# Performance work log

Measured on AMD Instinct MI355X. Metric: run time of the kernel, lower is better.

The kernel has to match this reference:

```python
import jax, jax.numpy as jnp
import numpy as np

B = 262144      # points per batch
DIM = 3         # input_dim
L = 16          # levels
T = 19          # log2 hash table size
F = 2           # features per level
N_MIN, N_MAX = 16, 512

_b = np.exp((np.log(N_MAX) - np.log(N_MIN)) / (L - 1))
RES = np.floor(N_MIN * _b ** np.arange(L)).astype(np.float32).reshape(1, 1, L, 1)

# voxel corner offsets [1, DIM, 1, 2^DIM]
_border = np.empty((DIM, 2 ** DIM), dtype=np.uint32)
for i in range(DIM):
    _border[i, :] = np.array(([0] * 2 ** i + [1] * 2 ** i) * 2 ** (DIM - i - 1), dtype=np.uint32)
BORDER = _border.reshape(1, DIM, 1, 2 ** DIM)

# tiny-cuda-nn hash primes; all fit in uint32. Since the torch code takes the
# result mod 2^T (a power of two), int64 and uint32 arithmetic agree on the
# low bits, so uint32 hashing is bit-exact with the original.
PRIMES = np.array([1, 2654435761, 805459861], dtype=np.uint32)
MASK = np.uint32(2 ** T - 1)


def setup_inputs() -> dict:
    key = jax.random.key(0)
    k1, k2 = jax.random.split(key)
    x = jax.random.uniform(k1, (B, DIM), dtype=jnp.float32)  # coords in [0,1)
    tables = jax.random.uniform(k2, (L, 2 ** T, F), dtype=jnp.float32,
                                minval=-1e-4, maxval=1e-4)
    return {"x": x, "tables": tables}


def reference(x, tables):
    res = jnp.asarray(RES)                                   # [1,1,L,1]
    border = jnp.asarray(BORDER)                             # [1,DIM,1,2^DIM]
    primes = jnp.asarray(PRIMES)
    scaled = x[:, :, None, None] * res                       # [B,DIM,L,1]
    grid = jnp.floor(scaled).astype(jnp.uint32) + border     # [B,DIM,L,2^DIM]
    # spatial hash: xor of per-dim coord * prime, mod 2^T
    h = (grid[:, 0] * primes[0]) ^ (grid[:, 1] * primes[1]) ^ (grid[:, 2] * primes[2])
    idx = (h & MASK).astype(jnp.int32)                       # [B,L,2^DIM]
    gathered = tables[jnp.arange(L)[None, :, None], idx]     # [B,L,2^DIM,F]
    # multilinear interpolation weights
    w = jnp.prod(1.0 - jnp.abs(scaled - grid.astype(scaled.dtype)), axis=1)  # [B,L,2^DIM]
    out = jnp.einsum('blv,blvf->blf', w, gathered)           # [B,L,F]
    return out.reshape(x.shape[0], L * F)
```

## Files before the change

### kernel.cpp

```cpp
#include <hip/hip_runtime.h>


#define NB 262144
#define NL 16
#define TSIZE (1u << 19)
#define TMASK ((1u << 19) - 1u)
#define P1 2654435761u
#define P2 805459861u
#define NBKT 32768

typedef float vf2 __attribute__((ext_vector_type(2)));
typedef float vf4 __attribute__((ext_vector_type(4)));

__constant__ float RES_C[NL] = {16.f, 20.f, 25.f, 32.f, 40.f, 50.f, 64.f, 80.f,
                                101.f, 128.f, 161.f, 203.f, 256.f, 322.f, 406.f, 512.f};

__constant__ int SEQ_C[NL] = {0, 15, 1, 14, 2, 13, 3, 12, 4, 11, 5, 10, 6, 9, 7, 8};

__device__ __forceinline__ int bucket_of(float px, float py, float pz) {
  int bx = min(31, (int)(px * 32.0f));
  int by = min(31, (int)(py * 32.0f));
  int bz = min(31, (int)(pz * 32.0f));
  return bx | (by << 5) | (bz << 10);
}

__device__ __forceinline__ void ngp_point_level(
    float px, float py, float pz, int l, const float* __restrict__ tables,
    float& o0, float& o1) {
  const float res = RES_C[l];
  const float sx = px * res, sy = py * res, sz = pz * res;
  const float fx = floorf(sx), fy = floorf(sy), fz = floorf(sz);
  const unsigned ix = (unsigned)fx, iy = (unsigned)fy, iz = (unsigned)fz;

  const unsigned hx0 = ix, hx1 = ix + 1u;
  const unsigned hy0 = iy * P1, hy1 = hy0 + P1;
  const unsigned hz0 = iz * P2, hz1 = hz0 + P2;

  const float wx0 = 1.0f - fabsf(sx - fx);
  const float wx1 = 1.0f - fabsf(sx - (fx + 1.0f));
  const float wy0 = 1.0f - fabsf(sy - fy);
  const float wy1 = 1.0f - fabsf(sy - (fy + 1.0f));
  const float wz0 = 1.0f - fabsf(sz - fz);
  const float wz1 = 1.0f - fabsf(sz - (fz + 1.0f));

  const vf2* __restrict__ tbl = (const vf2*)tables + (size_t)l * TSIZE;

  unsigned idxs[8];
#pragma unroll
  for (int v = 0; v < 8; ++v) {
    const unsigned hx = (v & 1) ? hx1 : hx0;
    const unsigned hy = (v & 2) ? hy1 : hy0;
    const unsigned hz = (v & 4) ? hz1 : hz0;
    idxs[v] = (hx ^ hy ^ hz) & TMASK;
  }
  vf2 g[8];
#pragma unroll
  for (int v = 0; v < 8; ++v) g[v] = tbl[idxs[v]];

  o0 = 0.0f; o1 = 0.0f;
#pragma unroll
  for (int v = 0; v < 8; ++v) {
    const float w = ((v & 1) ? wx1 : wx0) * ((v & 2) ? wy1 : wy0) * ((v & 4) ? wz1 : wz0);
    o0 = fmaf(w, g[v].x, o0);
    o1 = fmaf(w, g[v].y, o1);
  }
}

__global__ __launch_bounds__(256) void zero_kernel(unsigned* __restrict__ hist) {
  hist[blockIdx.x * 256 + threadIdx.x] = 0u;
}

__global__ __launch_bounds__(256) void hist_kernel(
    const float* __restrict__ x, unsigned* __restrict__ hist) {
  const int b = blockIdx.x * 256 + threadIdx.x;
  const float px = x[b * 3 + 0], py = x[b * 3 + 1], pz = x[b * 3 + 2];
  atomicAdd(&hist[bucket_of(px, py, pz)], 1u);
}

__global__ __launch_bounds__(1024) void scan_kernel(
    const unsigned* __restrict__ hist, unsigned* __restrict__ offs) {
  __shared__ unsigned part[1024];
  const int t = threadIdx.x;
  const int base = t * 32;
  unsigned loc[32];
  unsigned s = 0;
#pragma unroll
  for (int i = 0; i < 32; ++i) { loc[i] = s; s += hist[base + i]; }
  part[t] = s;
  __syncthreads();
  for (int d = 1; d < 1024; d <<= 1) {
    unsigned v = (t >= d) ? part[t - d] : 0u;
    __syncthreads();
    part[t] += v;
    __syncthreads();
  }
  const unsigned pre = (t == 0) ? 0u : part[t - 1];
#pragma unroll
  for (int i = 0; i < 32; ++i) offs[base + i] = pre + loc[i];
}

__global__ __launch_bounds__(256) void scatter_kernel(
    const float* __restrict__ x, unsigned* __restrict__ offs,
    vf4* __restrict__ xp) {
  const int b = blockIdx.x * 256 + threadIdx.x;
  const float px = x[b * 3 + 0], py = x[b * 3 + 1], pz = x[b * 3 + 2];
  const unsigned pos = atomicAdd(&offs[bucket_of(px, py, pz)], 1u);
  vf4 v; v.x = px; v.y = py; v.z = pz; v.w = __uint_as_float((unsigned)b);
  xp[pos] = v;
}

__global__ __launch_bounds__(256) void ngp_gather_sorted_kernel(
    const vf4* __restrict__ xp,
    const float* __restrict__ tables,
    vf2* __restrict__ ws) {
  const int i = blockIdx.x;
  const int lvl = SEQ_C[i >> 10];
  const int chunk = i & 1023;
  const int p = chunk * 256 + threadIdx.x;

  const vf4 v = __builtin_nontemporal_load(xp + p);

  float o0, o1;
  ngp_point_level(v.x, v.y, v.z, lvl, tables, o0, o1);

  vf2 r; r.x = o0; r.y = o1;
  __builtin_nontemporal_store(r, ws + (size_t)lvl * NB + p);
}

__global__ __launch_bounds__(256) void ngp_transpose_sorted_kernel(
    const vf2* __restrict__ ws,
    const vf4* __restrict__ xp,
    vf4* __restrict__ out4) {
  __shared__ vf2 tile[NL][257];
  __shared__ unsigned pid[256];
  const int t = threadIdx.x;
  const int p0 = blockIdx.x * 256;

#pragma unroll
  for (int l = 0; l < NL; ++l) {
    tile[l][t] = __builtin_nontemporal_load(ws + (size_t)l * NB + p0 + t);
  }
  pid[t] = __float_as_uint(xp[p0 + t].w);
  __syncthreads();

#pragma unroll
  for (int k = 0; k < 8; ++k) {
    const int q = k * 256 + t;
    const int pq = q >> 3;
    const int wq = q & 7;
    const vf2 a = tile[2 * wq + 0][pq];
    const vf2 c = tile[2 * wq + 1][pq];
    vf4 v; v.x = a.x; v.y = a.y; v.z = c.x; v.w = c.y;
    out4[(size_t)pid[pq] * 8 + wq] = v;
  }
}

__global__ __launch_bounds__(256) void ngp_gather_kernel(
    const float* __restrict__ x, const float* __restrict__ tables,
    vf2* __restrict__ ws) {
  const int i = blockIdx.x;
  const int lvl = (i & 7) | ((i >> 13) << 3);
  const int chunk = (i >> 3) & 1023;
  const int b = chunk * 256 + threadIdx.x;
  const float px = __builtin_nontemporal_load(x + b * 3 + 0);
  const float py = __builtin_nontemporal_load(x + b * 3 + 1);
  const float pz = __builtin_nontemporal_load(x + b * 3 + 2);
  float o0, o1;
  ngp_point_level(px, py, pz, lvl, tables, o0, o1);
  vf2 r; r.x = o0; r.y = o1;
  __builtin_nontemporal_store(r, ws + (size_t)lvl * NB + b);
}

__global__ __launch_bounds__(256) void ngp_transpose_kernel(
    const vf2* __restrict__ ws, vf4* __restrict__ out4) {
  __shared__ vf2 tile[NL][257];
  const int t = threadIdx.x;
  const int p0 = blockIdx.x * 256;
#pragma unroll
  for (int l = 0; l < NL; ++l) {
    tile[l][t] = __builtin_nontemporal_load(ws + (size_t)l * NB + p0 + t);
  }
  __syncthreads();
#pragma unroll
  for (int k = 0; k < 8; ++k) {
    const int q = k * 256 + t;
    const int pq = q >> 3;
    const int wq = q & 7;
    const vf2 a = tile[2 * wq + 0][pq];
    const vf2 c = tile[2 * wq + 1][pq];
    vf4 v; v.x = a.x; v.y = a.y; v.z = c.x; v.w = c.y;
    __builtin_nontemporal_store(v, out4 + (size_t)p0 * 8 + q);
  }
}

__global__ __launch_bounds__(256) void ngp_fused_kernel(
    const float* __restrict__ x, const float* __restrict__ tables,
    float* __restrict__ out) {
  const int tid = blockIdx.x * blockDim.x + threadIdx.x;
  const int l = tid & (NL - 1);
  const int b = tid >> 4;
  float o0, o1;
  ngp_point_level(x[b * 3], x[b * 3 + 1], x[b * 3 + 2], l, tables, o0, o1);
  float2 r = make_float2(o0, o1);
  ((float2*)out)[tid] = r;
}

extern "C" void kernel_launch(void* const* d_in, const int* in_sizes, int n_in,
                              void* d_out, int out_size, void* d_ws, size_t ws_size,
                              hipStream_t stream) {
  const float* x = (const float*)d_in[0];
  const float* tables = (const float*)d_in[1];
  float* out = (float*)d_out;

  const size_t ws2_b = (size_t)NL * NB * sizeof(vf2);
  const size_t xp_b = (size_t)NB * sizeof(vf4);
  const size_t hist_b = (size_t)NBKT * sizeof(unsigned);
  const size_t sorted_need = ws2_b + xp_b + 2 * hist_b;

  if (ws_size >= sorted_need) {
    char* base = (char*)d_ws;
    vf2* ws2 = (vf2*)base;
    vf4* xp = (vf4*)(base + ws2_b);
    unsigned* hist = (unsigned*)(base + ws2_b + xp_b);
    unsigned* offs = (unsigned*)(base + ws2_b + xp_b + hist_b);

    zero_kernel<<<NBKT / 256, 256, 0, stream>>>(hist);
    hist_kernel<<<NB / 256, 256, 0, stream>>>(x, hist);
    scan_kernel<<<1, 1024, 0, stream>>>(hist, offs);
    scatter_kernel<<<NB / 256, 256, 0, stream>>>(x, offs, xp);
    ngp_gather_sorted_kernel<<<NB * NL / 256, 256, 0, stream>>>(xp, tables, ws2);
    ngp_transpose_sorted_kernel<<<NB / 256, 256, 0, stream>>>(ws2, xp, (vf4*)out);
  } else if (ws_size >= ws2_b) {
    vf2* ws = (vf2*)d_ws;
    ngp_gather_kernel<<<NB * NL / 256, 256, 0, stream>>>(x, tables, ws);
    ngp_transpose_kernel<<<NB / 256, 256, 0, stream>>>(ws, (vf4*)out);
  } else {
    ngp_fused_kernel<<<NB * NL / 256, 256, 0, stream>>>(x, tables, out);
  }
}
```

Baseline: 204.7 us.

## Fuse histogram, scan and scatter into one kernel with a grid barrier

Replaces the zero, histogram, scan and scatter kernels with one sort kernel. It uses a global atomic spin barrier across all 1024 blocks, then has each block redundantly scan the histogram into shared memory before scattering. It also coarsens the spatial buckets from 32^3 to 16^3, so the per-block scan is cheaper. This removes several launches and the single-block scan, at the cost of relying on all 1024 blocks being co-resident and of coarser locality in the sorted order.

```diff
diff --git a/kernel.cpp b/kernel.cpp
--- a/kernel.cpp
+++ b/kernel.cpp
@@ -7,7 +7,8 @@
 #define TMASK ((1u << 19) - 1u)
 #define P1 2654435761u
 #define P2 805459861u
-#define NBKT 32768
+#define NBKT 4096
+#define SORT_BLOCKS 1024
 
 typedef float vf2 __attribute__((ext_vector_type(2)));
 typedef float vf4 __attribute__((ext_vector_type(4)));
@@ -18,10 +19,10 @@
 __constant__ int SEQ_C[NL] = {0, 15, 1, 14, 2, 13, 3, 12, 4, 11, 5, 10, 6, 9, 7, 8};
 
 __device__ __forceinline__ int bucket_of(float px, float py, float pz) {
-  int bx = min(31, (int)(px * 32.0f));
-  int by = min(31, (int)(py * 32.0f));
-  int bz = min(31, (int)(pz * 32.0f));
-  return bx | (by << 5) | (bz << 10);
+  int bx = min(15, (int)(px * 16.0f));
+  int by = min(15, (int)(py * 16.0f));
+  int bz = min(15, (int)(pz * 16.0f));
+  return bx | (by << 4) | (bz << 8);
 }
 
 __device__ __forceinline__ void ngp_point_level(
@@ -66,29 +67,43 @@
   }
 }
 
-__global__ __launch_bounds__(256) void zero_kernel(unsigned* __restrict__ hist) {
-  hist[blockIdx.x * 256 + threadIdx.x] = 0u;
-}
-
-__global__ __launch_bounds__(256) void hist_kernel(
-    const float* __restrict__ x, unsigned* __restrict__ hist) {
-  const int b = blockIdx.x * 256 + threadIdx.x;
+__global__ __launch_bounds__(256) void sort_kernel(
+    const float* __restrict__ x, unsigned* __restrict__ hist,
+    unsigned* __restrict__ cnt, unsigned* __restrict__ bar,
+    vf4* __restrict__ xp) {
+  __shared__ unsigned soff[NBKT];
+  __shared__ unsigned part[256];
+  const int t = threadIdx.x;
+  const int b = blockIdx.x * 256 + t;
+
   const float px = x[b * 3 + 0], py = x[b * 3 + 1], pz = x[b * 3 + 2];
-  atomicAdd(&hist[bucket_of(px, py, pz)], 1u);
-}
-
-__global__ __launch_bounds__(1024) void scan_kernel(
-    const unsigned* __restrict__ hist, unsigned* __restrict__ offs) {
-  __shared__ unsigned part[1024];
-  const int t = threadIdx.x;
-  const int base = t * 32;
-  unsigned loc[32];
+  const int bkt = bucket_of(px, py, pz);
+  atomicAdd(&hist[bkt], 1u);
+
+  __syncthreads();
+  if (t == 0) {
+    __threadfence();
+    atomicAdd(&bar[0], 1u);
+    while (__hip_atomic_load(&bar[0], __ATOMIC_RELAXED,
+                             __HIP_MEMORY_SCOPE_AGENT) < SORT_BLOCKS) {
+      __builtin_amdgcn_s_sleep(2);
+    }
+  }
+  __syncthreads();
+  __threadfence();
+
+  const int base = t * (NBKT / 256);
+  unsigned loc[NBKT / 256];
   unsigned s = 0;
 #pragma unroll
-  for (int i = 0; i < 32; ++i) { loc[i] = s; s += hist[base + i]; }
+  for (int i = 0; i < NBKT / 256; ++i) {
+    loc[i] = s;
+    s += __hip_atomic_load(&hist[base + i], __ATOMIC_RELAXED,
+                           __HIP_MEMORY_SCOPE_AGENT);
+  }
   part[t] = s;
   __syncthreads();
-  for (int d = 1; d < 1024; d <<= 1) {
+  for (int d = 1; d < 256; d <<= 1) {
     unsigned v = (t >= d) ? part[t - d] : 0u;
     __syncthreads();
     part[t] += v;
@@ -96,15 +111,11 @@
   }
   const unsigned pre = (t == 0) ? 0u : part[t - 1];
 #pragma unroll
-  for (int i = 0; i < 32; ++i) offs[base + i] = pre + loc[i];
-}
-
-__global__ __launch_bounds__(256) void scatter_kernel(
-    const float* __restrict__ x, unsigned* __restrict__ offs,
-    vf4* __restrict__ xp) {
-  const int b = blockIdx.x * 256 + threadIdx.x;
-  const float px = x[b * 3 + 0], py = x[b * 3 + 1], pz = x[b * 3 + 2];
-  const unsigned pos = atomicAdd(&offs[bucket_of(px, py, pz)], 1u);
+  for (int i = 0; i < NBKT / 256; ++i) soff[base + i] = pre + loc[i];
+  __syncthreads();
+
+  const unsigned rank = atomicAdd(&cnt[bkt], 1u);
+  const unsigned pos = soff[bkt] + rank;
   vf4 v; v.x = px; v.y = py; v.z = pz; v.w = __uint_as_float((unsigned)b);
   xp[pos] = v;
 }
@@ -215,19 +226,19 @@
   const size_t ws2_b = (size_t)NL * NB * sizeof(vf2);
   const size_t xp_b = (size_t)NB * sizeof(vf4);
   const size_t hist_b = (size_t)NBKT * sizeof(unsigned);
-  const size_t sorted_need = ws2_b + xp_b + 2 * hist_b;
+  const size_t bar_b = 256;
+  const size_t sorted_need = ws2_b + xp_b + 2 * hist_b + bar_b;
 
   if (ws_size >= sorted_need) {
     char* base = (char*)d_ws;
     vf2* ws2 = (vf2*)base;
     vf4* xp = (vf4*)(base + ws2_b);
     unsigned* hist = (unsigned*)(base + ws2_b + xp_b);
-    unsigned* offs = (unsigned*)(base + ws2_b + xp_b + hist_b);
-
-    zero_kernel<<<NBKT / 256, 256, 0, stream>>>(hist);
-    hist_kernel<<<NB / 256, 256, 0, stream>>>(x, hist);
-    scan_kernel<<<1, 1024, 0, stream>>>(hist, offs);
-    scatter_kernel<<<NB / 256, 256, 0, stream>>>(x, offs, xp);
+    unsigned* cnt = (unsigned*)(base + ws2_b + xp_b + hist_b);
+    unsigned* bar = (unsigned*)(base + ws2_b + xp_b + 2 * hist_b);
+
+    hipMemsetAsync(hist, 0, 2 * hist_b + bar_b, stream);
+    sort_kernel<<<SORT_BLOCKS, 256, 0, stream>>>(x, hist, cnt, bar, xp);
     ngp_gather_sorted_kernel<<<NB * NL / 256, 256, 0, stream>>>(xp, tables, ws2);
     ngp_transpose_sorted_kernel<<<NB / 256, 256, 0, stream>>>(ws2, xp, (vf4*)out);
   } else if (ws_size >= ws2_b) {
```

Result: slower. 331.2 us (+61.8%).
